# Kernel tuning notes

Hardware: AMD Instinct MI355X
Metric: run time of the kernel (lower is better)

Reference implementation:

```python
import jax, jax.numpy as jnp
import numpy as np

V, E, H, T = 8000, 256, 256, 4  # vocab, embed, lstm hidden, tagset (BMES)
B, S = 64, 512


def setup_inputs() -> dict:
    key = jax.random.key(0)
    ks = jax.random.split(key, 16)
    w = lambda k, shape, s=0.05: (jax.random.normal(k, shape, jnp.float32) * s)
    return {
        "sentence": jax.random.randint(ks[0], (B, S), 0, V),
        "tags": jax.random.randint(ks[1], (B, S), 0, T),
        "length_list": jnp.full((B,), S, dtype=jnp.int32),
        "emb": w(ks[2], (V, E), 0.1),
        "Wih_f": w(ks[3], (4 * H, E)), "Whh_f": w(ks[4], (4 * H, H)), "b_f": jnp.zeros((4 * H,), jnp.float32),
        "Wih_b": w(ks[5], (4 * H, E)), "Whh_b": w(ks[6], (4 * H, H)), "b_b": jnp.zeros((4 * H,), jnp.float32),
        "Wlin": w(ks[7], (T, 2 * H), 0.05), "blin": jnp.zeros((T,), jnp.float32),
        "start_trans": w(ks[8], (T,), 0.1), "end_trans": w(ks[9], (T,), 0.1),
        "transitions": w(ks[10], (T, T), 0.1),
    }


def _lstm_dir(xs, Wih, Whh, b, reverse):
    # xs: [S, B, E] time-major; PyTorch gate order i,f,g,o
    Bv, Hh = xs.shape[1], Whh.shape[1]
    def step(carry, x):
        h, c = carry
        g = x @ Wih.T + h @ Whh.T + b
        i, f, gg, o = jnp.split(g, 4, axis=-1)
        c = jax.nn.sigmoid(f) * c + jax.nn.sigmoid(i) * jnp.tanh(gg)
        h = jax.nn.sigmoid(o) * jnp.tanh(c)
        return (h, c), h
    init = (jnp.zeros((Bv, Hh), xs.dtype), jnp.zeros((Bv, Hh), xs.dtype))
    _, hs = jax.lax.scan(step, init, xs, reverse=reverse)
    return hs  # [S, B, H]


def _crf_llh(emis, tagsT, start, end, trans):
    # emis: [S, B, T] time-major; tagsT: [S, B]. No mask (matches original call).
    e_sc = jnp.take_along_axis(emis, tagsT[:, :, None], axis=2)[..., 0]  # [S, B]
    tr_sc = trans[tagsT[:-1], tagsT[1:]]                                  # [S-1, B]
    num = start[tagsT[0]] + e_sc.sum(0) + tr_sc.sum(0) + end[tagsT[-1]]   # [B]
    alpha = start[None, :] + emis[0]                                      # [B, T]
    def step(alpha, e):
        return jax.nn.logsumexp(alpha[:, :, None] + trans[None], axis=1) + e, None
    alpha, _ = jax.lax.scan(step, alpha, emis[1:])
    denom = jax.nn.logsumexp(alpha + end[None, :], axis=1)                # [B]
    return num - denom


def _viterbi(emis, start, end, trans):
    # emis: [S, B, T] -> best tag path [B, S]
    score = start[None, :] + emis[0]                                      # [B, T]
    def step(score, e):
        cand = score[:, :, None] + trans[None]                            # [B, T_prev, T_next]
        bp = jnp.argmax(cand, axis=1)                                     # [B, T]
        return jnp.max(cand, axis=1) + e, bp
    score, bps = jax.lax.scan(step, score, emis[1:])                      # bps: [S-1, B, T]
    last = jnp.argmax(score + end[None, :], axis=1)                       # [B]
    def back(tag, bp):
        prev = jnp.take_along_axis(bp, tag[:, None], axis=1)[:, 0]
        return prev, prev
    _, path = jax.lax.scan(back, last, bps, reverse=True)                 # [S-1, B]
    return jnp.concatenate([path, last[None]], axis=0).T                  # [B, S]


def reference(sentence, tags, length_list, emb, Wih_f, Whh_f, b_f,
              Wih_b, Whh_b, b_b, Wlin, blin, start_trans, end_trans, transitions):
    xs = jnp.swapaxes(emb[sentence], 0, 1)                                # [S, B, E]
    hf = _lstm_dir(xs, Wih_f, Whh_f, b_f, reverse=False)
    hb = _lstm_dir(xs, Wih_b, Whh_b, b_b, reverse=True)
    h = jnp.concatenate([hf, hb], axis=-1)                                # [S, B, 2H] (dropout = eval identity)
    emis = h @ Wlin.T + blin                                              # [S, B, T]
    loss = -jnp.sum(_crf_llh(emis, tags.T, start_trans, end_trans, transitions))
    tag_seq = _viterbi(emis, start_trans, end_trans, transitions)
    return tag_seq, loss
```

## Files before the change

kernel.cpp:

```cpp
#include <hip/hip_runtime.h>
#include <math.h>

#define Vv 8000
#define Ee 256
#define Hh 256
#define Tt 4
#define Bb 64
#define Ss 512

#define EPROJ_PER_DIR (Vv * 1024)
#define WMAT_PER_DIR  (Ee * 1024)

#define NSTAT 18
#define NSTRM 14
#define STAT_U32 (NSTAT * 512 * 4)

__device__ __forceinline__ float sigm(float x) { return 1.f / (1.f + expf(-x)); }

#if defined(__has_builtin)
# if __has_builtin(__builtin_amdgcn_sdot4)
#  define HAS_SDOT4 1
# endif
#endif

__device__ __forceinline__ int dot4i8(unsigned a, unsigned b, int c) {
#ifdef HAS_SDOT4
    return __builtin_amdgcn_sdot4((int)a, (int)b, c, false);
#else
    int s = c;
    #pragma unroll
    for (int i = 0; i < 4; ++i) {
        const int xa = ((int)(a << (24 - 8 * i))) >> 24;
        const int xb = ((int)(b << (24 - 8 * i))) >> 24;
        s += xa * xb;
    }
    return s;
#endif
}

__global__ void prep1_kernel(const float* __restrict__ Wih_f, const float* __restrict__ b_f,
                             const float* __restrict__ Wih_b, const float* __restrict__ b_b,
                             const float* __restrict__ Wlin,
                             float* __restrict__ WihP, float* __restrict__ bP,
                             float* __restrict__ WlinQ)
{
    int tid = blockIdx.x * blockDim.x + threadIdx.x;
    int dir = tid >> 18;
    int r   = tid & 262143;
    int k   = r >> 10;
    int jp  = r & 1023;
    int u   = jp >> 2;
    int g   = jp & 3;
    int row = g * 256 + u;
    const float* Wih = dir ? Wih_b : Wih_f;
    const float* bv  = dir ? b_b   : b_f;
    WihP[dir * WMAT_PER_DIR + k * 1024 + jp] = Wih[row * 256 + k];
    if (r < 1024) {
        bP[dir * 1024 + jp] = bv[row];
        int uu = r >> 2, tt = r & 3;
        WlinQ[(dir * 256 + uu) * 4 + tt] = Wlin[tt * (2 * Hh) + dir * 256 + uu];
    }
}

__global__ __launch_bounds__(256) void scale_kernel(const float* __restrict__ Whh_f,
                                                    const float* __restrict__ Whh_b,
                                                    float* __restrict__ scales)
{
    const int gw = blockIdx.x * 4 + (threadIdx.x >> 6);
    const int lane = threadIdx.x & 63;
    const int dir = gw >> 10;
    const int row = gw & 1023;
    const float* W = dir ? Whh_b : Whh_f;
    const float* src = W + (size_t)row * 256 + lane * 4;
    float m = fmaxf(fmaxf(fabsf(src[0]), fabsf(src[1])),
                    fmaxf(fabsf(src[2]), fabsf(src[3])));
    #pragma unroll
    for (int off = 32; off > 0; off >>= 1) m = fmaxf(m, __shfl_down(m, off));
    if (lane == 0) scales[gw] = fmaxf(m, 1e-12f) / 127.f;
}

__global__ __launch_bounds__(256) void quant_kernel(const float* __restrict__ Whh_f,
                                                    const float* __restrict__ Whh_b,
                                                    const float* __restrict__ scales,
                                                    unsigned int* __restrict__ W8)
{
    const int idx = blockIdx.x * 256 + threadIdx.x;
    const int dir = idx >> 16;
    const int rem = idx & 65535;
    int slot, t, j, kw;
    if (rem < STAT_U32) {
        slot = rem >> 11; const int r2 = rem & 2047; t = r2 >> 2; j = r2 & 3;
        kw = 2 * slot + (j >> 1);
    } else {
        const int q2 = rem - STAT_U32;
        slot = q2 >> 11; const int r2 = q2 & 2047; t = r2 >> 2; j = r2 & 3;
        kw = 36 + 2 * slot + (j >> 1);
    }
    const int rr = j & 1;
    const int u = t & 255;
    const int gs = (t < 256 ? 0 : 2) + rr;
    const int row = gs * 256 + u;
    const float* W = dir ? Whh_b : Whh_f;
    const float sc = scales[dir * 1024 + row];
    const float inv = 1.f / sc;
    unsigned int v = 0;
    #pragma unroll
    for (int i = 0; i < 4; ++i) {
        const float w = W[(size_t)row * 256 + kw * 4 + i];
        int q = (int)rintf(w * inv);
        q = q > 127 ? 127 : (q < -127 ? -127 : q);
        v |= ((unsigned int)(unsigned char)(signed char)q) << (8 * i);
    }
    W8[idx] = v;
}

__global__ __launch_bounds__(512) void wl8_kernel(const float* __restrict__ Wlin,
                                                  unsigned int* __restrict__ wl8T,
                                                  float* __restrict__ scfac)
{
    const int w = threadIdx.x >> 6;
    const int lane = threadIdx.x & 63;
    const int dir = w >> 2, t = w & 3;
    const float4 v = *(const float4*)(Wlin + t * (2 * Hh) + dir * 256 + lane * 4);
    float m = fmaxf(fmaxf(fabsf(v.x), fabsf(v.y)), fmaxf(fabsf(v.z), fabsf(v.w)));
    #pragma unroll
    for (int off = 32; off > 0; off >>= 1) m = fmaxf(m, __shfl_down(m, off));
    const float mall = __builtin_amdgcn_readfirstlane(m);
    const float sc = fmaxf(mall, 1e-12f) / 127.f;
    const float inv = 1.f / sc;
    const float vv[4] = {v.x, v.y, v.z, v.w};
    unsigned int pk = 0;
    #pragma unroll
    for (int i = 0; i < 4; ++i) {
        int q = (int)rintf(vv[i] * inv);
        q = q > 127 ? 127 : (q < -127 ? -127 : q);
        pk |= ((unsigned int)(unsigned char)(signed char)q) << (8 * i);
    }
    wl8T[w * 64 + lane] = pk;
    if (lane == 0) scfac[w] = sc / 127.f;
}

#define BM 64
#define BN 128
#define BK 16
__global__ __launch_bounds__(256) void embproj_gemm(const float* __restrict__ emb,
                                                    const float* __restrict__ WihP,
                                                    const float* __restrict__ bP,
                                                    float* __restrict__ embproj)
{
    int dir = blockIdx.z;
    const float* Bmat = WihP + dir * WMAT_PER_DIR;
    float* C = embproj + (size_t)dir * EPROJ_PER_DIR;
    int m0 = blockIdx.x * BM;
    int n0 = blockIdx.y * BN;

    __shared__ float As[BK][BM];
    __shared__ float Bs[BK][BN];

    int t = threadIdx.x;
    int tm = (t & 15) * 4;
    int tn = (t >> 4) * 8;
    float acc[4][8];
    #pragma unroll
    for (int i = 0; i < 4; ++i)
        #pragma unroll
        for (int j = 0; j < 8; ++j) acc[i][j] = 0.f;

    for (int k0 = 0; k0 < Ee; k0 += BK) {
        {
            int row = t >> 2, seg = t & 3;
            float4 a4 = *(const float4*)(&emb[(size_t)(m0 + row) * Ee + k0 + seg * 4]);
            As[seg * 4 + 0][row] = a4.x;
            As[seg * 4 + 1][row] = a4.y;
            As[seg * 4 + 2][row] = a4.z;
            As[seg * 4 + 3][row] = a4.w;
        }
        {
            int kk = t >> 4, nn = (t & 15) * 8;
            float4 b0 = *(const float4*)(&Bmat[(size_t)(k0 + kk) * 1024 + n0 + nn]);
            float4 b1 = *(const float4*)(&Bmat[(size_t)(k0 + kk) * 1024 + n0 + nn + 4]);
            *(float4*)&Bs[kk][nn]     = b0;
            *(float4*)&Bs[kk][nn + 4] = b1;
        }
        __syncthreads();
        #pragma unroll
        for (int k = 0; k < BK; ++k) {
            float4 a  = *(const float4*)&As[k][tm];
            float4 b0 = *(const float4*)&Bs[k][tn];
            float4 b1 = *(const float4*)&Bs[k][tn + 4];
            float av[4] = {a.x, a.y, a.z, a.w};
            float bv[8] = {b0.x, b0.y, b0.z, b0.w, b1.x, b1.y, b1.z, b1.w};
            #pragma unroll
            for (int i = 0; i < 4; ++i)
                #pragma unroll
                for (int j = 0; j < 8; ++j)
                    acc[i][j] += av[i] * bv[j];
        }
        __syncthreads();
    }
    #pragma unroll
    for (int i = 0; i < 4; ++i) {
        int m = m0 + tm + i;
        #pragma unroll
        for (int j = 0; j < 8; j += 4) {
            float4 o;
            o.x = acc[i][j + 0] + bP[dir * 1024 + n0 + tn + j + 0];
            o.y = acc[i][j + 1] + bP[dir * 1024 + n0 + tn + j + 1];
            o.z = acc[i][j + 2] + bP[dir * 1024 + n0 + tn + j + 2];
            o.w = acc[i][j + 3] + bP[dir * 1024 + n0 + tn + j + 3];
            *(float4*)&C[(size_t)m * 1024 + n0 + tn + j] = o;
        }
    }
}

__global__ __attribute__((amdgpu_flat_work_group_size(512, 512)))
__attribute__((amdgpu_waves_per_eu(2, 2))) void lstm_stream_kernel(
    const int* __restrict__ sentence,
    const float* __restrict__ embproj,
    const unsigned int* __restrict__ W8,
    const float* __restrict__ scales,
    const unsigned int* __restrict__ wl8T,
    const float* __restrict__ scfac,
    float* __restrict__ emisP)
{
    extern __shared__ char smem[];
    uint4*        SWl   = (uint4*)smem;
    unsigned int* h8    = (unsigned int*)(smem + 147456);
    float2*       part  = (float2*)(smem + 147456 + 256);

    const int bx  = blockIdx.x;
    const int dir = bx >> 6;
    const int b   = bx & 63;
    const int t   = threadIdx.x;
    const int lane = t & 63, wv = t >> 6;
    const int u   = t & 255;
    const bool lo = (t < 256);
    const int gs0 = lo ? 0 : 2;

    const unsigned int* Wd   = W8 + (size_t)dir * 65536;
    const unsigned int* Wstr = Wd + STAT_U32;

    #pragma unroll
    for (int i = 0; i < NSTAT; ++i)
        SWl[i * 512 + t] = *(const uint4*)(Wd + (size_t)(i * 512 + t) * 4);
    if (t < 64) h8[t] = 0u;

    const float sc0 = scales[dir * 1024 + gs0 * 256 + u] * (1.f / 127.f);
    const float sc1 = scales[dir * 1024 + (gs0 + 1) * 256 + u] * (1.f / 127.f);
    const float* EP = embproj + (size_t)dir * EPROJ_PER_DIR;
    const int* sent = sentence + (size_t)b * Ss;
    float c = 0.f;

    unsigned int wlq0 = 0, wlq1 = 0, wlq2 = 0, wlq3 = 0;
    float4 efac = make_float4(0.f, 0.f, 0.f, 0.f);
    if (wv == 4) {
        wlq0 = wl8T[(dir * 4 + 0) * 64 + lane];
        wlq1 = wl8T[(dir * 4 + 1) * 64 + lane];
        wlq2 = wl8T[(dir * 4 + 2) * 64 + lane];
        wlq3 = wl8T[(dir * 4 + 3) * 64 + lane];
        efac = *(const float4*)&scfac[dir * 4];
    }

    __syncthreads();

    for (int s = 0; s < Ss; ++s) {
        const int pos = dir ? (Ss - 1 - s) : s;
        const int tok = sent[pos];
        const float2 ep = *(const float2*)(EP + (size_t)tok * 1024 + u * 4 + gs0);

        const int v_h = (int)h8[lane];

        uint4 sb[NSTRM];
        #pragma unroll
        for (int i = 0; i < NSTRM; ++i)
            sb[i] = *(const uint4*)(Wstr + (size_t)(i * 512 + t) * 4);

        if (wv == 4 && s > 0) {
            int e0 = dot4i8(wlq0, (unsigned)v_h, 0);
            int e1 = dot4i8(wlq1, (unsigned)v_h, 0);
            int e2 = dot4i8(wlq2, (unsigned)v_h, 0);
            int e3 = dot4i8(wlq3, (unsigned)v_h, 0);
            #pragma unroll
            for (int off = 32; off > 0; off >>= 1) {
                e0 += __shfl_down(e0, off); e1 += __shfl_down(e1, off);
                e2 += __shfl_down(e2, off); e3 += __shfl_down(e3, off);
            }
            if (lane == 0) {
                const int pp = dir ? (Ss - s) : (s - 1);
                float4 o;
                o.x = (float)e0 * efac.x; o.y = (float)e1 * efac.y;
                o.z = (float)e2 * efac.z; o.w = (float)e3 * efac.w;
                *(float4*)&emisP[(((size_t)dir * Ss + pp) * Bb + b) * 4] = o;
            }
        }

        int a0e = 0, a1e = 0, a0o = 0, a1o = 0;
        #pragma unroll
        for (int i = 0; i < NSTAT; ++i) {
            const uint4 w = SWl[i * 512 + t];
            const unsigned h0 = (unsigned)__builtin_amdgcn_readlane(v_h, 2 * i);
            const unsigned h1 = (unsigned)__builtin_amdgcn_readlane(v_h, 2 * i + 1);
            if (i & 1) {
                a0o = dot4i8(w.x, h0, a0o); a1o = dot4i8(w.y, h0, a1o);
                a0o = dot4i8(w.z, h1, a0o); a1o = dot4i8(w.w, h1, a1o);
            } else {
                a0e = dot4i8(w.x, h0, a0e); a1e = dot4i8(w.y, h0, a1e);
                a0e = dot4i8(w.z, h1, a0e); a1e = dot4i8(w.w, h1, a1e);
            }
        }
        #pragma unroll
        for (int i = 0; i < NSTRM; ++i) {
            const uint4 w = sb[i];
            const unsigned h0 = (unsigned)__builtin_amdgcn_readlane(v_h, 36 + 2 * i);
            const unsigned h1 = (unsigned)__builtin_amdgcn_readlane(v_h, 37 + 2 * i);
            if (i & 1) {
                a0o = dot4i8(w.x, h0, a0o); a1o = dot4i8(w.y, h0, a1o);
                a0o = dot4i8(w.z, h1, a0o); a1o = dot4i8(w.w, h1, a1o);
            } else {
                a0e = dot4i8(w.x, h0, a0e); a1e = dot4i8(w.y, h0, a1e);
                a0e = dot4i8(w.z, h1, a0e); a1e = dot4i8(w.w, h1, a1e);
            }
        }
        const int a0 = a0e + a0o, a1 = a1e + a1o;

        const float g0 = (float)a0 * sc0 + ep.x;
        const float g1 = (float)a1 * sc1 + ep.y;
        if (!lo) part[u] = make_float2(g0, g1);
        __syncthreads();

        if (lo) {
            const float2 pg = part[u];
            c = sigm(g1) * c + sigm(g0) * tanhf(pg.x);
            const float h = sigm(pg.y) * tanhf(c);
            ((char*)h8)[u] = (char)(int)rintf(h * 127.f);
        }
        __syncthreads();
    }

    if (wv == 4) {
        const int v_h = (int)h8[lane];
        int e0 = dot4i8(wlq0, (unsigned)v_h, 0);
        int e1 = dot4i8(wlq1, (unsigned)v_h, 0);
        int e2 = dot4i8(wlq2, (unsigned)v_h, 0);
        int e3 = dot4i8(wlq3, (unsigned)v_h, 0);
        #pragma unroll
        for (int off = 32; off > 0; off >>= 1) {
            e0 += __shfl_down(e0, off); e1 += __shfl_down(e1, off);
            e2 += __shfl_down(e2, off); e3 += __shfl_down(e3, off);
        }
        if (lane == 0) {
            const int pp = dir ? 0 : (Ss - 1);
            float4 o;
            o.x = (float)e0 * efac.x; o.y = (float)e1 * efac.y;
            o.z = (float)e2 * efac.z; o.w = (float)e3 * efac.w;
            *(float4*)&emisP[(((size_t)dir * Ss + pp) * Bb + b) * 4] = o;
        }
    }
}

#define EM2(S_, B_, J_) (emisA[(((size_t)(S_)) * Bb + (B_)) * 4 + (J_)] + \
                         emisB[(((size_t)(S_)) * Bb + (B_)) * 4 + (J_)])

__global__ __launch_bounds__(64) void tail_kernel(
    const float* __restrict__ emisA, const float* __restrict__ emisB,
    const float* __restrict__ blin, const float* __restrict__ start_t,
    const float* __restrict__ end_t, const float* __restrict__ trans,
    const int* __restrict__ tags, float* __restrict__ out_tags,
    float* __restrict__ out_loss)
{
    const int blk = blockIdx.x;
    const int t = threadIdx.x;
    const int b_loc = t >> 2, j = t & 3;
    const int base = t & ~3;

    if (blk < 4) {
        __shared__ unsigned char bp_sh[16][513][4];
        __shared__ unsigned char tag_sh[16][520];
        const int b = blk * 16 + b_loc;
        const float trj0 = trans[0*4+j], trj1 = trans[1*4+j],
                    trj2 = trans[2*4+j], trj3 = trans[3*4+j];
        const float blj = blin[j];
        float score = start_t[j] + EM2(0, b, j) + blj;
        for (int s = 1; s < Ss; ++s) {
            const float e = EM2(s, b, j) + blj;
            const float s0 = __shfl(score, base+0), s1 = __shfl(score, base+1),
                        s2 = __shfl(score, base+2), s3 = __shfl(score, base+3);
            float best = s0 + trj0; int bi = 0;
            float v = s1 + trj1; if (v > best) { best = v; bi = 1; }
            v = s2 + trj2; if (v > best) { best = v; bi = 2; }
            v = s3 + trj3; if (v > best) { best = v; bi = 3; }
            score = best + e;
            bp_sh[b_loc][s][j] = (unsigned char)bi;
        }
        const float fv = score + end_t[j];
        const float f0 = __shfl(fv, base+0), f1 = __shfl(fv, base+1),
                    f2 = __shfl(fv, base+2), f3 = __shfl(fv, base+3);
        __syncthreads();
        if (j == 0) {
            float best = f0; int tag = 0;
            if (f1 > best) { best = f1; tag = 1; }
            if (f2 > best) { best = f2; tag = 2; }
            if (f3 > best) { best = f3; tag = 3; }
            tag_sh[b_loc][Ss-1] = (unsigned char)tag;
            for (int s = Ss - 1; s >= 1; --s) {
                tag = bp_sh[b_loc][s][tag];
                tag_sh[b_loc][s-1] = (unsigned char)tag;
            }
        }
        __syncthreads();
        for (int idx = t; idx < 16 * Ss; idx += 64) {
            const int bl = idx >> 9, s = idx & (Ss - 1);
            out_tags[(size_t)(blk*16 + bl) * Ss + s] = (float)tag_sh[bl][s];
        }
    } else {
        const int b = (blk - 4) * 16 + b_loc;
        const float trj0 = trans[0*4+j], trj1 = trans[1*4+j],
                    trj2 = trans[2*4+j], trj3 = trans[3*4+j];
        const float blj = blin[j];
        float alpha = start_t[j] + EM2(0, b, j) + blj;
        for (int s = 1; s < Ss; ++s) {
            const float e = EM2(s, b, j) + blj;
            const float a0 = __shfl(alpha, base+0), a1 = __shfl(alpha, base+1),
                        a2 = __shfl(alpha, base+2), a3 = __shfl(alpha, base+3);
            const float x0 = a0 + trj0, x1 = a1 + trj1, x2 = a2 + trj2, x3 = a3 + trj3;
            const float m = fmaxf(fmaxf(x0, x1), fmaxf(x2, x3));
            alpha = m + logf(expf(x0-m) + expf(x1-m) + expf(x2-m) + expf(x3-m)) + e;
        }
        const float dv = alpha + end_t[j];
        const float d0 = __shfl(dv, base+0), d1 = __shfl(dv, base+1),
                    d2 = __shfl(dv, base+2), d3 = __shfl(dv, base+3);
        const float dm = fmaxf(fmaxf(d0, d1), fmaxf(d2, d3));
        const float denom = dm + logf(expf(d0-dm) + expf(d1-dm) + expf(d2-dm) + expf(d3-dm));

        const int lo = j * 128, hi = lo + 128;
        float num = 0.f;
        int tprev = (lo > 0) ? tags[(size_t)b*Ss + lo - 1] : 0;
        if (j == 0) num += start_t[tags[(size_t)b*Ss]];
        if (j == 3) num += end_t[tags[(size_t)b*Ss + Ss - 1]];
        for (int s = lo; s < hi; ++s) {
            const int tg = tags[(size_t)b*Ss + s];
            num += EM2(s, b, tg) + blin[tg];
            if (s > 0) num += trans[tprev*4 + tg];
            tprev = tg;
        }
        num += __shfl_xor(num, 1);
        num += __shfl_xor(num, 2);
        float lb = (j == 0) ? (denom - num) : 0.f;
        #pragma unroll
        for (int off = 32; off > 0; off >>= 1) lb += __shfl_down(lb, off);
        if (t == 0) atomicAdd(out_loss, lb);
    }
}

extern "C" void kernel_launch(void* const* d_in, const int* in_sizes, int n_in,
                              void* d_out, int out_size, void* d_ws, size_t ws_size,
                              hipStream_t stream)
{
    const int*   sentence = (const int*)d_in[0];
    const int*   tags     = (const int*)d_in[1];
    const float* emb      = (const float*)d_in[3];
    const float* Wih_f    = (const float*)d_in[4];
    const float* Whh_f    = (const float*)d_in[5];
    const float* b_f      = (const float*)d_in[6];
    const float* Wih_b    = (const float*)d_in[7];
    const float* Whh_b    = (const float*)d_in[8];
    const float* b_b      = (const float*)d_in[9];
    const float* Wlin     = (const float*)d_in[10];
    const float* blin     = (const float*)d_in[11];
    const float* start_t  = (const float*)d_in[12];
    const float* end_t    = (const float*)d_in[13];
    const float* trans    = (const float*)d_in[14];

    float*        embproj = (float*)d_ws;
    float*        WihP    = embproj + 2 * EPROJ_PER_DIR;
    float*        bP      = WihP + 2 * WMAT_PER_DIR;
    float*        WlinQ   = bP + 2048;
    float*        scales  = WlinQ + 2048;
    unsigned int* W8      = (unsigned int*)(scales + 2048);
    unsigned int* wl8T    = W8 + 131072;
    float*        scfac   = (float*)(wl8T + 512);
    float*        emisP   = scfac + 56;
    float*        emisA   = emisP;
    float*        emisB   = emisP + Ss * Bb * 4;

    prep1_kernel<<<2048, 256, 0, stream>>>(Wih_f, b_f, Wih_b, b_b, Wlin,
                                           WihP, bP, WlinQ);
    scale_kernel<<<512, 256, 0, stream>>>(Whh_f, Whh_b, scales);
    quant_kernel<<<512, 256, 0, stream>>>(Whh_f, Whh_b, scales, W8);
    wl8_kernel<<<1, 512, 0, stream>>>(Wlin, wl8T, scfac);

    dim3 gg(Vv / BM, 1024 / BN, 2);
    embproj_gemm<<<gg, 256, 0, stream>>>(emb, WihP, bP, embproj);

    lstm_stream_kernel<<<128, 512, 149760, stream>>>(sentence, embproj, W8,
                                                     scales, wl8T, scfac, emisP);

    float* out = (float*)d_out;
    float* out_loss = out + Bb * Ss;
    hipMemsetAsync(out_loss, 0, sizeof(float), stream);
    tail_kernel<<<8, 64, 0, stream>>>(emisA, emisB, blin, start_t, end_t, trans,
                                      tags, out, out_loss);
}
```

Measured before the change: 1.064 ms.

## Keep streamed recurrent weights in registers and pair gates via lane shuffles

Moves most of the int8 recurrent weight matrix out of LDS into per-thread registers loaded once before the time loop (NSTAT 18→8, NSTRM 24), instead of re-reading the streamed part from global memory every step. Gate rows are re-interleaved so adjacent lanes hold complementary gates, which are exchanged with __shfl_xor instead of an LDS partial buffer. The hidden-state buffer is double-buffered, removing one __syncthreads per step. This raises register pressure (24 uint4 per thread) and risks spills, and it shrinks LDS use.

Measured after the change: 1.062 ms. About the same (-0.1%).

```diff
diff --git a/kernel.cpp b/kernel.cpp
--- a/kernel.cpp
+++ b/kernel.cpp
@@ -11,8 +11,8 @@
 #define EPROJ_PER_DIR (Vv * 1024)
 #define WMAT_PER_DIR  (Ee * 1024)
 
-#define NSTAT 18
-#define NSTRM 14
+#define NSTAT 8
+#define NSTRM 24
 #define STAT_U32 (NSTAT * 512 * 4)
 
 __device__ __forceinline__ float sigm(float x) { return 1.f / (1.f + expf(-x)); }
@@ -94,11 +94,11 @@
     } else {
         const int q2 = rem - STAT_U32;
         slot = q2 >> 11; const int r2 = q2 & 2047; t = r2 >> 2; j = r2 & 3;
-        kw = 36 + 2 * slot + (j >> 1);
+        kw = 2 * NSTAT + 2 * slot + (j >> 1);
     }
     const int rr = j & 1;
-    const int u = t & 255;
-    const int gs = (t < 256 ? 0 : 2) + rr;
+    const int u  = t >> 1;
+    const int gs = (t & 1) * 2 + rr;
     const int row = gs * 256 + u;
     const float* W = dir ? Whh_b : Whh_f;
     const float sc = scales[dir * 1024 + row];
@@ -224,18 +224,17 @@
     float* __restrict__ emisP)
 {
     extern __shared__ char smem[];
-    uint4*        SWl   = (uint4*)smem;
-    unsigned int* h8    = (unsigned int*)(smem + 147456);
-    float2*       part  = (float2*)(smem + 147456 + 256);
+    uint4*        SWl = (uint4*)smem;
+    unsigned int* h8  = (unsigned int*)(smem + STAT_U32*4);
 
     const int bx  = blockIdx.x;
     const int dir = bx >> 6;
     const int b   = bx & 63;
     const int t   = threadIdx.x;
     const int lane = t & 63, wv = t >> 6;
-    const int u   = t & 255;
-    const bool lo = (t < 256);
-    const int gs0 = lo ? 0 : 2;
+    const int u    = t >> 1;
+    const int gs0  = (t & 1) * 2;
+    const bool ev  = !(t & 1);
 
     const unsigned int* Wd   = W8 + (size_t)dir * 65536;
     const unsigned int* Wstr = Wd + STAT_U32;
@@ -243,9 +242,14 @@
     #pragma unroll
     for (int i = 0; i < NSTAT; ++i)
         SWl[i * 512 + t] = *(const uint4*)(Wd + (size_t)(i * 512 + t) * 4);
-    if (t < 64) h8[t] = 0u;
-
-    const float sc0 = scales[dir * 1024 + gs0 * 256 + u] * (1.f / 127.f);
+    if (t < 128) h8[t] = 0u;
+
+    uint4 sb[NSTRM];
+    #pragma unroll
+    for (int i = 0; i < NSTRM; ++i)
+        sb[i] = *(const uint4*)(Wstr + (size_t)(i * 512 + t) * 4);
+
+    const float sc0 = scales[dir * 1024 + (gs0 + 0) * 256 + u] * (1.f / 127.f);
     const float sc1 = scales[dir * 1024 + (gs0 + 1) * 256 + u] * (1.f / 127.f);
     const float* EP = embproj + (size_t)dir * EPROJ_PER_DIR;
     const int* sent = sentence + (size_t)b * Ss;
@@ -268,12 +272,9 @@
         const int tok = sent[pos];
         const float2 ep = *(const float2*)(EP + (size_t)tok * 1024 + u * 4 + gs0);
 
-        const int v_h = (int)h8[lane];
-
-        uint4 sb[NSTRM];
-        #pragma unroll
-        for (int i = 0; i < NSTRM; ++i)
-            sb[i] = *(const uint4*)(Wstr + (size_t)(i * 512 + t) * 4);
+        const int rp = (s + 1) & 1;
+        const int wp = s & 1;
+        const int v_h = (int)h8[rp * 64 + lane];
 
         if (wv == 4 && s > 0) {
             int e0 = dot4i8(wlq0, (unsigned)v_h, 0);
@@ -311,8 +312,8 @@
         #pragma unroll
         for (int i = 0; i < NSTRM; ++i) {
             const uint4 w = sb[i];
-            const unsigned h0 = (unsigned)__builtin_amdgcn_readlane(v_h, 36 + 2 * i);
-            const unsigned h1 = (unsigned)__builtin_amdgcn_readlane(v_h, 37 + 2 * i);
+            const unsigned h0 = (unsigned)__builtin_amdgcn_readlane(v_h, 2 * NSTAT + 2 * i);
+            const unsigned h1 = (unsigned)__builtin_amdgcn_readlane(v_h, 2 * NSTAT + 2 * i + 1);
             if (i & 1) {
                 a0o = dot4i8(w.x, h0, a0o); a1o = dot4i8(w.y, h0, a1o);
                 a0o = dot4i8(w.z, h1, a0o); a1o = dot4i8(w.w, h1, a1o);
@@ -325,20 +326,18 @@
 
         const float g0 = (float)a0 * sc0 + ep.x;
         const float g1 = (float)a1 * sc1 + ep.y;
-        if (!lo) part[u] = make_float2(g0, g1);
+        const float pg0 = __shfl_xor(g0, 1);
+        const float pg1 = __shfl_xor(g1, 1);
+        if (ev) {
+            c = sigm(g1) * c + sigm(g0) * tanhf(pg0);
+            const float h = sigm(pg1) * tanhf(c);
+            ((char*)h8)[wp * 256 + u] = (char)(int)rintf(h * 127.f);
+        }
         __syncthreads();
-
-        if (lo) {
-            const float2 pg = part[u];
-            c = sigm(g1) * c + sigm(g0) * tanhf(pg.x);
-            const float h = sigm(pg.y) * tanhf(c);
-            ((char*)h8)[u] = (char)(int)rintf(h * 127.f);
-        }
-        __syncthreads();
     }
 
     if (wv == 4) {
-        const int v_h = (int)h8[lane];
+        const int v_h = (int)h8[((Ss - 1) & 1) * 64 + lane];
         int e0 = dot4i8(wlq0, (unsigned)v_h, 0);
         int e1 = dot4i8(wlq1, (unsigned)v_h, 0);
         int e2 = dot4i8(wlq2, (unsigned)v_h, 0);
@@ -492,8 +491,8 @@
     dim3 gg(Vv / BM, 1024 / BN, 2);
     embproj_gemm<<<gg, 256, 0, stream>>>(emb, WihP, bP, embproj);
 
-    lstm_stream_kernel<<<128, 512, 149760, stream>>>(sentence, embproj, W8,
-                                                     scales, wl8T, scfac, emisP);
+    lstm_stream_kernel<<<128, 512, STAT_U32 * 4 + 512, stream>>>(
+        sentence, embproj, W8, scales, wl8T, scfac, emisP);
 
     float* out = (float*)d_out;
     float* out_loss = out + Bb * Ss;
```
